# Kernel optimization log

Measured on AMD Instinct MI355X. Metric: run time of the kernel, lower is better.

Reference implementation:

```python
import jax, jax.numpy as jnp
import numpy as np

N = 100000   # nodes
E = 1600000  # edges
G = 512      # graphs in batch
IN_C, H1, H2, OUT_C = 3, 64, 128, 2


def setup_inputs() -> dict:
    key = jax.random.key(0)
    ks = jax.random.split(key, 9)
    x = jax.random.normal(ks[0], (N, IN_C), dtype=jnp.float32)
    edge_index = jax.random.randint(ks[1], (2, E), 0, N, dtype=jnp.int64)
    batch = jnp.sort(jax.random.randint(ks[2], (N,), 0, G, dtype=jnp.int64))
    # Glorot-ish init for weights, zeros for biases (as PyG GCNConv / nn.Linear defaults roughly)
    def glorot(k, shape):
        lim = float(np.sqrt(6.0 / (shape[0] + shape[1])))
        return jax.random.uniform(k, shape, jnp.float32, -lim, lim)
    W1 = glorot(ks[3], (IN_C, H1)); b1 = jnp.zeros((H1,), jnp.float32)
    W2 = glorot(ks[4], (H1, H2));   b2 = jnp.zeros((H2,), jnp.float32)
    Wfc = glorot(ks[5], (H2, OUT_C)); bfc = jnp.zeros((OUT_C,), jnp.float32)
    return {"x": x, "edge_index": edge_index, "batch": batch,
            "W1": W1, "b1": b1, "W2": W2, "b2": b2, "Wfc": Wfc, "bfc": bfc}


def _gcn_conv(x, W, b, src, dst, dinv):
    # PyG GCNConv: out = D^{-1/2} (A + I) D^{-1/2} X W + b
    xw = x @ W                                    # [N, F]
    norm = dinv[src] * dinv[dst]                  # per-edge symmetric norm
    agg = jax.ops.segment_sum(norm[:, None] * xw[src], dst, num_segments=x.shape[0])
    agg = agg + (dinv * dinv)[:, None] * xw       # self-loop contribution
    return agg + b


def reference(x, edge_index, batch, W1, b1, W2, b2, Wfc, bfc):
    src, dst = edge_index[0], edge_index[1]
    # degree with self-loops (edge weight 1), counted at edge targets as in PyG
    deg = jax.ops.segment_sum(jnp.ones((E,), x.dtype), dst, num_segments=N) + 1.0
    dinv = jax.lax.rsqrt(deg)
    h = jax.nn.relu(_gcn_conv(x, W1, b1, src, dst, dinv))
    h = jax.nn.relu(_gcn_conv(h, W2, b2, src, dst, dinv))
    # global_mean_pool over batch indices
    sums = jax.ops.segment_sum(h, batch, num_segments=G)          # [G, H2]
    cnt = jax.ops.segment_sum(jnp.ones((N,), h.dtype), batch, num_segments=G)
    pooled = sums / jnp.maximum(cnt, 1.0)[:, None]
    return pooled @ Wfc + bfc
```

## Files before the change

kernel.cpp:

```cpp
#include <hip/hip_runtime.h>

#define NN 100000
#define NE 1600000
#define NG 512
#define C_H1 64
#define C_H2 128
#define C_OUT 2

#define MM2_BLOCKS ((NN + 63) / 64)
#define NB ((NN + 255) >> 8)
#define PCHUNKS 512
#define PCHUNK_E (NE / PCHUNKS)

__global__ void k_hist(const int* __restrict__ ei, int* __restrict__ hist) {
    __shared__ int lh[NB];
    int tid = threadIdx.x;
    int blk = blockIdx.x;
    for (int i = tid; i < NB; i += 256) lh[i] = 0;
    __syncthreads();
    int base = blk * PCHUNK_E;
    for (int e = base + tid; e < base + PCHUNK_E; e += 256)
        atomicAdd(&lh[ei[NE + e] >> 8], 1);
    __syncthreads();
    for (int i = tid; i < NB; i += 256) hist[i * PCHUNKS + blk] = lh[i];
}

__global__ void k_colscan0(const int* __restrict__ hist, int* __restrict__ offs,
                           int* __restrict__ btot) {
    __shared__ int sh[256];
    int b = blockIdx.x;
    int tid = threadIdx.x;
    int v0 = hist[b * PCHUNKS + 2 * tid];
    int v1 = hist[b * PCHUNKS + 2 * tid + 1];
    sh[tid] = v0 + v1;
    __syncthreads();
    for (int off = 1; off < 256; off <<= 1) {
        int v = (tid >= off) ? sh[tid - off] : 0;
        __syncthreads();
        sh[tid] += v;
        __syncthreads();
    }
    int base = (tid == 0) ? 0 : sh[tid - 1];
    offs[b * PCHUNKS + 2 * tid]     = base;
    offs[b * PCHUNKS + 2 * tid + 1] = base + v0;
    if (tid == 255) btot[b] = sh[255];
}

__global__ void k_bbase(const int* __restrict__ btot, int* __restrict__ bbase,
                        int* __restrict__ row_ptr) {
    __shared__ int sh[256];
    int tid = threadIdx.x;
    int v0 = (2 * tid     < NB) ? btot[2 * tid]     : 0;
    int v1 = (2 * tid + 1 < NB) ? btot[2 * tid + 1] : 0;
    sh[tid] = v0 + v1;
    __syncthreads();
    for (int off = 1; off < 256; off <<= 1) {
        int v = (tid >= off) ? sh[tid - off] : 0;
        __syncthreads();
        sh[tid] += v;
        __syncthreads();
    }
    int base = (tid == 0) ? 0 : sh[tid - 1];
    if (2 * tid     < NB) bbase[2 * tid]     = base;
    if (2 * tid + 1 < NB) bbase[2 * tid + 1] = base + v0;
    if (tid == 255) { bbase[NB] = sh[255]; row_ptr[NN] = sh[255]; }
}

__global__ void k_scatterA(const int* __restrict__ ei, const int* __restrict__ offs,
                           const int* __restrict__ bbase, int2* __restrict__ ed2) {
    __shared__ int lcur[NB];
    int tid = threadIdx.x;
    int blk = blockIdx.x;
    for (int i = tid; i < NB; i += 256) lcur[i] = bbase[i] + offs[i * PCHUNKS + blk];
    __syncthreads();
    int base = blk * PCHUNK_E;
    for (int e = base + tid; e < base + PCHUNK_E; e += 256) {
        int s = ei[e], d = ei[NE + e];
        int pos = atomicAdd(&lcur[d >> 8], 1);
        int2 v; v.x = s; v.y = d;
        ed2[pos] = v;
    }
}

__global__ void k_B1(const int2* __restrict__ ed2, const int* __restrict__ bbase,
                     float* __restrict__ dinv, int* __restrict__ row_ptr) {
    __shared__ int ldeg[256];
    __shared__ int sh[256];
    int b = blockIdx.x;
    int tid = threadIdx.x;
    int lo = b << 8;
    ldeg[tid] = 0;
    __syncthreads();
    int beg = bbase[b], end = bbase[b + 1];
    for (int j = beg + tid; j < end; j += 256)
        atomicAdd(&ldeg[ed2[j].y - lo], 1);
    __syncthreads();
    int d = ldeg[tid];
    int node = lo + tid;
    if (node < NN) dinv[node] = rsqrtf((float)d + 1.0f);
    sh[tid] = d;
    __syncthreads();
    for (int off = 1; off < 256; off <<= 1) {
        int v = (tid >= off) ? sh[tid - off] : 0;
        __syncthreads();
        sh[tid] += v;
        __syncthreads();
    }
    int excl = beg + ((tid == 0) ? 0 : sh[tid - 1]);
    if (node < NN) row_ptr[node] = excl;
}

__global__ void k_scatterB(const int* __restrict__ row_ptr, const int2* __restrict__ ed2,
                           const float* __restrict__ dinv, int2* __restrict__ ed) {
    __shared__ int   lcur[256];
    __shared__ float ldin[256];
    int b = blockIdx.x;
    int lo = b << 8;
    int tid = threadIdx.x;
    int node = lo + tid;
    if (node <= NN) lcur[tid] = row_ptr[node < NN ? node : NN];
    else            lcur[tid] = 0;
    ldin[tid] = (node < NN) ? dinv[node] : 0.f;
    __syncthreads();
    int seg_beg = row_ptr[lo];
    int hi = lo + 256; if (hi > NN) hi = NN;
    int seg_end = row_ptr[hi];
    for (int j = seg_beg + tid; j < seg_end; j += 256) {
        int2 sd = ed2[j];
        int local = sd.y - lo;
        int pos = atomicAdd(&lcur[local], 1);
        int2 v; v.x = sd.x; v.y = __float_as_int(dinv[sd.x] * ldin[local]);
        ed[pos] = v;
    }
}

__global__ void k_aggx(const int* __restrict__ row_ptr, const int2* __restrict__ ed,
                       const float* __restrict__ dinv, const float* __restrict__ x,
                       float* __restrict__ aggx) {
    int n = blockIdx.x * blockDim.x + threadIdx.x;
    if (n >= NN) return;
    float di = dinv[n];
    float s2 = di * di;
    float a0 = s2 * x[n * 3], a1 = s2 * x[n * 3 + 1], a2 = s2 * x[n * 3 + 2];
    int beg = row_ptr[n], end = row_ptr[n + 1];
    for (int j = beg; j < end; ++j) {
        int2 v = ed[j];
        float w = __int_as_float(v.y);
        const float* xs = x + v.x * 3;
        a0 = fmaf(w, xs[0], a0);
        a1 = fmaf(w, xs[1], a1);
        a2 = fmaf(w, xs[2], a2);
    }
    aggx[n * 3]     = a0;
    aggx[n * 3 + 1] = a1;
    aggx[n * 3 + 2] = a2;
}

__global__ void k_pay(const int2* __restrict__ ed, const float* __restrict__ aggx,
                      float4* __restrict__ pay) {
    int j = blockIdx.x * 256 + threadIdx.x;
    int2 v = ed[j];
    const float* a = aggx + v.x * 3;
    float4 p;
    p.x = a[0]; p.y = a[1]; p.z = a[2];
    p.w = __int_as_float(v.y);
    pay[j] = p;
}

__global__ void k_edge1(const int* __restrict__ row_ptr, const float4* __restrict__ pay,
                        const float* __restrict__ aggx, const float* __restrict__ dinv,
                        const float* __restrict__ W1, const float* __restrict__ b1,
                        float* __restrict__ agg1) {
    __shared__ float4 lp[256];
    int t = blockIdx.x * 256 + threadIdx.x;
    int n = t >> 6, c = t & 63;
    int lane = threadIdx.x & 63;
    int wbase = threadIdx.x & 192;

    float w0 = W1[c], w1 = W1[64 + c], w2 = W1[128 + c], bb = b1[c];
    float a0 = aggx[n * 3], a1 = aggx[n * 3 + 1], a2 = aggx[n * 3 + 2];
    float di = dinv[n];
    float hself = fmaxf(fmaf(a0, w0, fmaf(a1, w1, fmaf(a2, w2, bb))), 0.f);
    float acc = di * di * hself;

    int beg = row_ptr[n], end = row_ptr[n + 1];
    for (int base = beg; base < end; base += 64) {
        int m = end - base; if (m > 64) m = 64;
        if (lane < m) lp[wbase + lane] = pay[base + lane];
        int e = 0;
        for (; e + 3 < m; e += 4) {
            float4 p0 = lp[wbase + e];
            float4 p1 = lp[wbase + e + 1];
            float4 p2 = lp[wbase + e + 2];
            float4 p3 = lp[wbase + e + 3];
            float h0 = fmaxf(fmaf(p0.x, w0, fmaf(p0.y, w1, fmaf(p0.z, w2, bb))), 0.f);
            float h1v = fmaxf(fmaf(p1.x, w0, fmaf(p1.y, w1, fmaf(p1.z, w2, bb))), 0.f);
            float h2v = fmaxf(fmaf(p2.x, w0, fmaf(p2.y, w1, fmaf(p2.z, w2, bb))), 0.f);
            float h3v = fmaxf(fmaf(p3.x, w0, fmaf(p3.y, w1, fmaf(p3.z, w2, bb))), 0.f);
            acc = fmaf(p0.w, h0, acc);
            acc = fmaf(p1.w, h1v, acc);
            acc = fmaf(p2.w, h2v, acc);
            acc = fmaf(p3.w, h3v, acc);
        }
        for (; e < m; ++e) {
            float4 p = lp[wbase + e];
            float h = fmaxf(fmaf(p.x, w0, fmaf(p.y, w1, fmaf(p.z, w2, bb))), 0.f);
            acc = fmaf(p.w, h, acc);
        }
    }
    agg1[t] = acc;
}

__global__ void k_mm2pool(const float* __restrict__ agg1, const float* __restrict__ W2,
                          const float* __restrict__ b2, const int* __restrict__ batch,
                          float* __restrict__ pooled) {
    __shared__ float wt[C_H1 * C_H2];
    __shared__ float at[64 * C_H1];
    int tid = threadIdx.x;
    {
        const float4* w4 = (const float4*)W2;
        float4* wl = (float4*)wt;
        for (int i = tid; i < (C_H1 * C_H2) / 4; i += 256) wl[i] = w4[i];
        const float4* a4 = (const float4*)(agg1 + (size_t)blockIdx.x * 64 * C_H1);
        float4* al = (float4*)at;
        for (int i = tid; i < (64 * C_H1) / 4; i += 256) al[i] = a4[i];
    }
    __syncthreads();

    int tx = tid & 31;
    int my = tid >> 5;
    int c0 = tx * 4;
    int m0 = my * 8;

    float acc[8][4];
#pragma unroll
    for (int i = 0; i < 8; ++i)
#pragma unroll
        for (int j = 0; j < 4; ++j) acc[i][j] = 0.f;

    for (int k0 = 0; k0 < C_H1; k0 += 4) {
        float4 wf[4];
#pragma unroll
        for (int kk = 0; kk < 4; ++kk)
            wf[kk] = *(const float4*)&wt[(k0 + kk) * C_H2 + c0];
#pragma unroll
        for (int i = 0; i < 8; ++i) {
            float4 af = *(const float4*)&at[(m0 + i) * C_H1 + k0];
            acc[i][0] = fmaf(af.x, wf[0].x, acc[i][0]);
            acc[i][1] = fmaf(af.x, wf[0].y, acc[i][1]);
            acc[i][2] = fmaf(af.x, wf[0].z, acc[i][2]);
            acc[i][3] = fmaf(af.x, wf[0].w, acc[i][3]);
            acc[i][0] = fmaf(af.y, wf[1].x, acc[i][0]);
            acc[i][1] = fmaf(af.y, wf[1].y, acc[i][1]);
            acc[i][2] = fmaf(af.y, wf[1].z, acc[i][2]);
            acc[i][3] = fmaf(af.y, wf[1].w, acc[i][3]);
            acc[i][0] = fmaf(af.z, wf[2].x, acc[i][0]);
            acc[i][1] = fmaf(af.z, wf[2].y, acc[i][1]);
            acc[i][2] = fmaf(af.z, wf[2].z, acc[i][2]);
            acc[i][3] = fmaf(af.z, wf[2].w, acc[i][3]);
            acc[i][0] = fmaf(af.w, wf[3].x, acc[i][0]);
            acc[i][1] = fmaf(af.w, wf[3].y, acc[i][1]);
            acc[i][2] = fmaf(af.w, wf[3].z, acc[i][2]);
            acc[i][3] = fmaf(af.w, wf[3].w, acc[i][3]);
        }
    }

    int nbase = blockIdx.x * 64 + m0;
    int gidx[8];
#pragma unroll
    for (int i = 0; i < 8; ++i)
        gidx[i] = (nbase + i < NN) ? batch[nbase + i] : -1;
    float bias[4];
#pragma unroll
    for (int j = 0; j < 4; ++j) bias[j] = b2[c0 + j];

#pragma unroll
    for (int j = 0; j < 4; ++j) {
        int run_g = -1;
        float rs = 0.f;
#pragma unroll
        for (int i = 0; i < 8; ++i) {
            if (gidx[i] < 0) break;
            float h = fmaxf(acc[i][j] + bias[j], 0.f);
            if (gidx[i] != run_g) {
                if (run_g >= 0) atomicAdd(&pooled[(run_g << 7) + c0 + j], rs);
                run_g = gidx[i]; rs = h;
            } else {
                rs += h;
            }
        }
        if (run_g >= 0) atomicAdd(&pooled[(run_g << 7) + c0 + j], rs);
    }
}

__device__ __forceinline__ int lower_bound(const int* __restrict__ a, int n, int key) {
    int lo = 0, hi = n;
    while (lo < hi) { int mid = (lo + hi) >> 1; if (a[mid] < key) lo = mid + 1; else hi = mid; }
    return lo;
}

__global__ void k_fc(const float* __restrict__ pooled, const int* __restrict__ batch,
                     const float* __restrict__ Wfc, const float* __restrict__ bfc,
                     float* __restrict__ out) {
    int t = blockIdx.x * blockDim.x + threadIdx.x;
    if (t >= NG * C_OUT) return;
    int g = t >> 1, o = t & 1;
    int start = lower_bound(batch, NN, g);
    int end   = lower_bound(batch, NN, g + 1);
    float inv = 1.f / fmaxf((float)(end - start), 1.f);
    float s = bfc[o];
    for (int cc = 0; cc < C_H2; ++cc)
        s = fmaf(pooled[(g << 7) + cc] * inv, Wfc[cc * C_OUT + o], s);
    out[t] = s;
}

extern "C" void kernel_launch(void* const* d_in, const int* in_sizes, int n_in,
                              void* d_out, int out_size, void* d_ws, size_t ws_size,
                              hipStream_t stream) {
    const float* x     = (const float*)d_in[0];
    const int*   ei    = (const int*)d_in[1];
    const int*   batch = (const int*)d_in[2];
    const float* W1    = (const float*)d_in[3];
    const float* b1    = (const float*)d_in[4];
    const float* W2    = (const float*)d_in[5];
    const float* b2    = (const float*)d_in[6];
    const float* Wfc   = (const float*)d_in[7];
    const float* bfc   = (const float*)d_in[8];
    float* out = (float*)d_out;

    char* p = (char*)d_ws;
    auto alloc = [&](size_t bytes) { char* r = p; p += (bytes + 255) & ~size_t(255); return r; };
    float*  dinv    = (float*) alloc((size_t)NN * 4);
    int*    row_ptr = (int*)   alloc((size_t)(NN + 1) * 4);
    int*    btot    = (int*)   alloc((size_t)NB * 4);
    int*    bbase   = (int*)   alloc((size_t)(NB + 1) * 4);
    int*    hist    = (int*)   alloc((size_t)NB * PCHUNKS * 4);
    int*    offs    = (int*)   alloc((size_t)NB * PCHUNKS * 4);
    int2*   ed2     = (int2*)  alloc((size_t)NE * 8);
    int2*   ed      = (int2*)  alloc((size_t)NE * 8);
    float*  aggx    = (float*) alloc((size_t)NN * 3 * 4);
    float4* pay     = (float4*)alloc((size_t)NE * 16);
    float*  agg1    = (float*) alloc((size_t)(NN + 64) * C_H1 * 4);
    float*  pooled  = (float*) alloc((size_t)NG * C_H2 * 4);

    hipMemsetAsync(pooled, 0, (size_t)NG * C_H2 * 4, stream);
    k_hist    <<<PCHUNKS, 256, 0, stream>>>(ei, hist);
    k_colscan0<<<NB, 256, 0, stream>>>(hist, offs, btot);
    k_bbase   <<<1, 256, 0, stream>>>(btot, bbase, row_ptr);
    k_scatterA<<<PCHUNKS, 256, 0, stream>>>(ei, offs, bbase, ed2);
    k_B1      <<<NB, 256, 0, stream>>>(ed2, bbase, dinv, row_ptr);
    k_scatterB<<<NB, 256, 0, stream>>>(row_ptr, ed2, dinv, ed);
    k_aggx    <<<(NN + 255) / 256, 256, 0, stream>>>(row_ptr, ed, dinv, x, aggx);
    k_pay     <<<NE / 256, 256, 0, stream>>>(ed, aggx, pay);
    k_edge1   <<<(NN * C_H1) / 256, 256, 0, stream>>>(row_ptr, pay, aggx, dinv, W1, b1, agg1);
    k_mm2pool <<<MM2_BLOCKS, 256, 0, stream>>>(agg1, W2, b2, batch, pooled);
    k_fc      <<<(NG * C_OUT + 255) / 256, 256, 0, stream>>>(pooled, batch, Wfc, bfc, out);
}
```

Baseline: 244.1 us.

## Fuse first-layer aggregation into CSR scatter and gather neighbors directly in edge kernel

The layer-1 input aggregation now runs inside the CSR scatter kernel using shared-memory float atomics, with x padded to float4. This removes the separate k_aggx pass. The materialised per-edge payload buffer (k_pay) is also dropped: k_edge1 now gathers aggx4 rows by edge source index on the fly, avoiding a 25.6MB write and read. The mm2pool kernel processes two 64-row tiles per block, so W2 is loaded into shared memory half as often. The costs are LDS atomic contention in the scatter, random gathers in edge1, and the float summation order changing from run to run.

Result: no change. 241.9 us (-0.9%).

```diff
diff --git a/kernel.cpp b/kernel.cpp
--- a/kernel.cpp
+++ b/kernel.cpp
@@ -7,7 +7,7 @@
 #define C_H2 128
 #define C_OUT 2
 
-#define MM2_BLOCKS ((NN + 63) / 64)
+#define MM2_BLOCKS ((NN + 127) / 128)
 #define NB ((NN + 255) >> 8)
 #define PCHUNKS 512
 #define PCHUNK_E (NE / PCHUNKS)
@@ -110,10 +110,19 @@
     if (node < NN) row_ptr[node] = excl;
 }
 
+__global__ void k_x4(const float* __restrict__ x, float4* __restrict__ x4) {
+    int n = blockIdx.x * blockDim.x + threadIdx.x;
+    if (n >= NN) return;
+    float4 v; v.x = x[n * 3]; v.y = x[n * 3 + 1]; v.z = x[n * 3 + 2]; v.w = 0.f;
+    x4[n] = v;
+}
+
 __global__ void k_scatterB(const int* __restrict__ row_ptr, const int2* __restrict__ ed2,
-                           const float* __restrict__ dinv, int2* __restrict__ ed) {
+                           const float* __restrict__ dinv, const float4* __restrict__ x4,
+                           int2* __restrict__ ed, float4* __restrict__ aggx4) {
     __shared__ int   lcur[256];
     __shared__ float ldin[256];
+    __shared__ float lax[256 * 3];
     int b = blockIdx.x;
     int lo = b << 8;
     int tid = threadIdx.x;
@@ -121,6 +130,7 @@
     if (node <= NN) lcur[tid] = row_ptr[node < NN ? node : NN];
     else            lcur[tid] = 0;
     ldin[tid] = (node < NN) ? dinv[node] : 0.f;
+    lax[tid] = 0.f; lax[256 + tid] = 0.f; lax[512 + tid] = 0.f;
     __syncthreads();
     int seg_beg = row_ptr[lo];
     int hi = lo + 256; if (hi > NN) hi = NN;
@@ -129,46 +139,30 @@
         int2 sd = ed2[j];
         int local = sd.y - lo;
         int pos = atomicAdd(&lcur[local], 1);
-        int2 v; v.x = sd.x; v.y = __float_as_int(dinv[sd.x] * ldin[local]);
+        float nrm = dinv[sd.x] * ldin[local];
+        int2 v; v.x = sd.x; v.y = __float_as_int(nrm);
         ed[pos] = v;
-    }
-}
-
-__global__ void k_aggx(const int* __restrict__ row_ptr, const int2* __restrict__ ed,
-                       const float* __restrict__ dinv, const float* __restrict__ x,
-                       float* __restrict__ aggx) {
-    int n = blockIdx.x * blockDim.x + threadIdx.x;
-    if (n >= NN) return;
-    float di = dinv[n];
-    float s2 = di * di;
-    float a0 = s2 * x[n * 3], a1 = s2 * x[n * 3 + 1], a2 = s2 * x[n * 3 + 2];
-    int beg = row_ptr[n], end = row_ptr[n + 1];
-    for (int j = beg; j < end; ++j) {
-        int2 v = ed[j];
-        float w = __int_as_float(v.y);
-        const float* xs = x + v.x * 3;
-        a0 = fmaf(w, xs[0], a0);
-        a1 = fmaf(w, xs[1], a1);
-        a2 = fmaf(w, xs[2], a2);
-    }
-    aggx[n * 3]     = a0;
-    aggx[n * 3 + 1] = a1;
-    aggx[n * 3 + 2] = a2;
-}
-
-__global__ void k_pay(const int2* __restrict__ ed, const float* __restrict__ aggx,
-                      float4* __restrict__ pay) {
-    int j = blockIdx.x * 256 + threadIdx.x;
-    int2 v = ed[j];
-    const float* a = aggx + v.x * 3;
-    float4 p;
-    p.x = a[0]; p.y = a[1]; p.z = a[2];
-    p.w = __int_as_float(v.y);
-    pay[j] = p;
-}
-
-__global__ void k_edge1(const int* __restrict__ row_ptr, const float4* __restrict__ pay,
-                        const float* __restrict__ aggx, const float* __restrict__ dinv,
+        float4 xs = x4[sd.x];
+        atomicAdd(&lax[local],       nrm * xs.x);
+        atomicAdd(&lax[256 + local], nrm * xs.y);
+        atomicAdd(&lax[512 + local], nrm * xs.z);
+    }
+    __syncthreads();
+    if (node < NN) {
+        float di = ldin[tid];
+        float s2 = di * di;
+        float4 xs = x4[node];
+        float4 a;
+        a.x = lax[tid]       + s2 * xs.x;
+        a.y = lax[256 + tid] + s2 * xs.y;
+        a.z = lax[512 + tid] + s2 * xs.z;
+        a.w = 0.f;
+        aggx4[node] = a;
+    }
+}
+
+__global__ void k_edge1(const int* __restrict__ row_ptr, const int2* __restrict__ ed,
+                        const float4* __restrict__ aggx4, const float* __restrict__ dinv,
                         const float* __restrict__ W1, const float* __restrict__ b1,
                         float* __restrict__ agg1) {
     __shared__ float4 lp[256];
@@ -178,22 +172,27 @@
     int wbase = threadIdx.x & 192;
 
     float w0 = W1[c], w1 = W1[64 + c], w2 = W1[128 + c], bb = b1[c];
-    float a0 = aggx[n * 3], a1 = aggx[n * 3 + 1], a2 = aggx[n * 3 + 2];
+    float4 an = aggx4[n];
     float di = dinv[n];
-    float hself = fmaxf(fmaf(a0, w0, fmaf(a1, w1, fmaf(a2, w2, bb))), 0.f);
+    float hself = fmaxf(fmaf(an.x, w0, fmaf(an.y, w1, fmaf(an.z, w2, bb))), 0.f);
     float acc = di * di * hself;
 
     int beg = row_ptr[n], end = row_ptr[n + 1];
     for (int base = beg; base < end; base += 64) {
         int m = end - base; if (m > 64) m = 64;
-        if (lane < m) lp[wbase + lane] = pay[base + lane];
+        if (lane < m) {
+            int2 v = ed[base + lane];
+            float4 ax = aggx4[v.x];
+            float4 p; p.x = ax.x; p.y = ax.y; p.z = ax.z; p.w = __int_as_float(v.y);
+            lp[wbase + lane] = p;
+        }
         int e = 0;
         for (; e + 3 < m; e += 4) {
             float4 p0 = lp[wbase + e];
             float4 p1 = lp[wbase + e + 1];
             float4 p2 = lp[wbase + e + 2];
             float4 p3 = lp[wbase + e + 3];
-            float h0 = fmaxf(fmaf(p0.x, w0, fmaf(p0.y, w1, fmaf(p0.z, w2, bb))), 0.f);
+            float h0  = fmaxf(fmaf(p0.x, w0, fmaf(p0.y, w1, fmaf(p0.z, w2, bb))), 0.f);
             float h1v = fmaxf(fmaf(p1.x, w0, fmaf(p1.y, w1, fmaf(p1.z, w2, bb))), 0.f);
             float h2v = fmaxf(fmaf(p2.x, w0, fmaf(p2.y, w1, fmaf(p2.z, w2, bb))), 0.f);
             float h3v = fmaxf(fmaf(p3.x, w0, fmaf(p3.y, w1, fmaf(p3.z, w2, bb))), 0.f);
@@ -221,75 +220,80 @@
         const float4* w4 = (const float4*)W2;
         float4* wl = (float4*)wt;
         for (int i = tid; i < (C_H1 * C_H2) / 4; i += 256) wl[i] = w4[i];
-        const float4* a4 = (const float4*)(agg1 + (size_t)blockIdx.x * 64 * C_H1);
-        float4* al = (float4*)at;
-        for (int i = tid; i < (64 * C_H1) / 4; i += 256) al[i] = a4[i];
-    }
-    __syncthreads();
-
+    }
     int tx = tid & 31;
     int my = tid >> 5;
     int c0 = tx * 4;
     int m0 = my * 8;
-
-    float acc[8][4];
-#pragma unroll
-    for (int i = 0; i < 8; ++i)
-#pragma unroll
-        for (int j = 0; j < 4; ++j) acc[i][j] = 0.f;
-
-    for (int k0 = 0; k0 < C_H1; k0 += 4) {
-        float4 wf[4];
-#pragma unroll
-        for (int kk = 0; kk < 4; ++kk)
-            wf[kk] = *(const float4*)&wt[(k0 + kk) * C_H2 + c0];
-#pragma unroll
-        for (int i = 0; i < 8; ++i) {
-            float4 af = *(const float4*)&at[(m0 + i) * C_H1 + k0];
-            acc[i][0] = fmaf(af.x, wf[0].x, acc[i][0]);
-            acc[i][1] = fmaf(af.x, wf[0].y, acc[i][1]);
-            acc[i][2] = fmaf(af.x, wf[0].z, acc[i][2]);
-            acc[i][3] = fmaf(af.x, wf[0].w, acc[i][3]);
-            acc[i][0] = fmaf(af.y, wf[1].x, acc[i][0]);
-            acc[i][1] = fmaf(af.y, wf[1].y, acc[i][1]);
-            acc[i][2] = fmaf(af.y, wf[1].z, acc[i][2]);
-            acc[i][3] = fmaf(af.y, wf[1].w, acc[i][3]);
-            acc[i][0] = fmaf(af.z, wf[2].x, acc[i][0]);
-            acc[i][1] = fmaf(af.z, wf[2].y, acc[i][1]);
-            acc[i][2] = fmaf(af.z, wf[2].z, acc[i][2]);
-            acc[i][3] = fmaf(af.z, wf[2].w, acc[i][3]);
-            acc[i][0] = fmaf(af.w, wf[3].x, acc[i][0]);
-            acc[i][1] = fmaf(af.w, wf[3].y, acc[i][1]);
-            acc[i][2] = fmaf(af.w, wf[3].z, acc[i][2]);
-            acc[i][3] = fmaf(af.w, wf[3].w, acc[i][3]);
-        }
-    }
-
-    int nbase = blockIdx.x * 64 + m0;
-    int gidx[8];
-#pragma unroll
-    for (int i = 0; i < 8; ++i)
-        gidx[i] = (nbase + i < NN) ? batch[nbase + i] : -1;
     float bias[4];
 #pragma unroll
     for (int j = 0; j < 4; ++j) bias[j] = b2[c0 + j];
 
-#pragma unroll
-    for (int j = 0; j < 4; ++j) {
-        int run_g = -1;
-        float rs = 0.f;
-#pragma unroll
-        for (int i = 0; i < 8; ++i) {
-            if (gidx[i] < 0) break;
-            float h = fmaxf(acc[i][j] + bias[j], 0.f);
-            if (gidx[i] != run_g) {
-                if (run_g >= 0) atomicAdd(&pooled[(run_g << 7) + c0 + j], rs);
-                run_g = gidx[i]; rs = h;
-            } else {
-                rs += h;
+    for (int tile = 0; tile < 2; ++tile) {
+        {
+            const float4* a4 = (const float4*)(agg1 + ((size_t)blockIdx.x * 128 + tile * 64) * C_H1);
+            float4* al = (float4*)at;
+            for (int i = tid; i < (64 * C_H1) / 4; i += 256) al[i] = a4[i];
+        }
+        __syncthreads();
+
+        float acc[8][4];
+#pragma unroll
+        for (int i = 0; i < 8; ++i)
+#pragma unroll
+            for (int j = 0; j < 4; ++j) acc[i][j] = 0.f;
+
+        for (int k0 = 0; k0 < C_H1; k0 += 4) {
+            float4 wf[4];
+#pragma unroll
+            for (int kk = 0; kk < 4; ++kk)
+                wf[kk] = *(const float4*)&wt[(k0 + kk) * C_H2 + c0];
+#pragma unroll
+            for (int i = 0; i < 8; ++i) {
+                float4 af = *(const float4*)&at[(m0 + i) * C_H1 + k0];
+                acc[i][0] = fmaf(af.x, wf[0].x, acc[i][0]);
+                acc[i][1] = fmaf(af.x, wf[0].y, acc[i][1]);
+                acc[i][2] = fmaf(af.x, wf[0].z, acc[i][2]);
+                acc[i][3] = fmaf(af.x, wf[0].w, acc[i][3]);
+                acc[i][0] = fmaf(af.y, wf[1].x, acc[i][0]);
+                acc[i][1] = fmaf(af.y, wf[1].y, acc[i][1]);
+                acc[i][2] = fmaf(af.y, wf[1].z, acc[i][2]);
+                acc[i][3] = fmaf(af.y, wf[1].w, acc[i][3]);
+                acc[i][0] = fmaf(af.z, wf[2].x, acc[i][0]);
+                acc[i][1] = fmaf(af.z, wf[2].y, acc[i][1]);
+                acc[i][2] = fmaf(af.z, wf[2].z, acc[i][2]);
+                acc[i][3] = fmaf(af.z, wf[2].w, acc[i][3]);
+                acc[i][0] = fmaf(af.w, wf[3].x, acc[i][0]);
+                acc[i][1] = fmaf(af.w, wf[3].y, acc[i][1]);
+                acc[i][2] = fmaf(af.w, wf[3].z, acc[i][2]);
+                acc[i][3] = fmaf(af.w, wf[3].w, acc[i][3]);
             }
         }
-        if (run_g >= 0) atomicAdd(&pooled[(run_g << 7) + c0 + j], rs);
+
+        int nbase = blockIdx.x * 128 + tile * 64 + m0;
+        int gidx[8];
+#pragma unroll
+        for (int i = 0; i < 8; ++i)
+            gidx[i] = (nbase + i < NN) ? batch[nbase + i] : -1;
+
+#pragma unroll
+        for (int j = 0; j < 4; ++j) {
+            int run_g = -1;
+            float rs = 0.f;
+#pragma unroll
+            for (int i = 0; i < 8; ++i) {
+                if (gidx[i] < 0) break;
+                float h = fmaxf(acc[i][j] + bias[j], 0.f);
+                if (gidx[i] != run_g) {
+                    if (run_g >= 0) atomicAdd(&pooled[(run_g << 7) + c0 + j], rs);
+                    run_g = gidx[i]; rs = h;
+                } else {
+                    rs += h;
+                }
+            }
+            if (run_g >= 0) atomicAdd(&pooled[(run_g << 7) + c0 + j], rs);
+        }
+        __syncthreads();
     }
 }
 
@@ -338,9 +342,9 @@
     int*    offs    = (int*)   alloc((size_t)NB * PCHUNKS * 4);
     int2*   ed2     = (int2*)  alloc((size_t)NE * 8);
     int2*   ed      = (int2*)  alloc((size_t)NE * 8);
-    float*  aggx    = (float*) alloc((size_t)NN * 3 * 4);
-    float4* pay     = (float4*)alloc((size_t)NE * 16);
-    float*  agg1    = (float*) alloc((size_t)(NN + 64) * C_H1 * 4);
+    float4* x4      = (float4*)alloc((size_t)NN * 16);
+    float4* aggx4   = (float4*)alloc((size_t)NN * 16);
+    float*  agg1    = (float*) alloc((size_t)(NN + 128) * C_H1 * 4);
     float*  pooled  = (float*) alloc((size_t)NG * C_H2 * 4);
 
     hipMemsetAsync(pooled, 0, (size_t)NG * C_H2 * 4, stream);
@@ -349,10 +353,9 @@
     k_bbase   <<<1, 256, 0, stream>>>(btot, bbase, row_ptr);
     k_scatterA<<<PCHUNKS, 256, 0, stream>>>(ei, offs, bbase, ed2);
     k_B1      <<<NB, 256, 0, stream>>>(ed2, bbase, dinv, row_ptr);
-    k_scatterB<<<NB, 256, 0, stream>>>(row_ptr, ed2, dinv, ed);
-    k_aggx    <<<(NN + 255) / 256, 256, 0, stream>>>(row_ptr, ed, dinv, x, aggx);
-    k_pay     <<<NE / 256, 256, 0, stream>>>(ed, aggx, pay);
-    k_edge1   <<<(NN * C_H1) / 256, 256, 0, stream>>>(row_ptr, pay, aggx, dinv, W1, b1, agg1);
+    k_x4      <<<(NN + 255) / 256, 256, 0, stream>>>(x, x4);
+    k_scatterB<<<NB, 256, 0, stream>>>(row_ptr, ed2, dinv, x4, ed, aggx4);
+    k_edge1   <<<(NN * C_H1) / 256, 256, 0, stream>>>(row_ptr, ed, aggx4, dinv, W1, b1, agg1);
     k_mm2pool <<<MM2_BLOCKS, 256, 0, stream>>>(agg1, W2, b2, batch, pooled);
     k_fc      <<<(NG * C_OUT + 255) / 256, 256, 0, stream>>>(pooled, batch, Wfc, bfc, out);
 }
```
